# Kernel optimization log

Measured on AMD Instinct MI355X. Metric: run time of the kernel, lower is better.

Reference implementation:

```python
import jax, jax.numpy as jnp
import numpy as np

N_HEADS = 8
HEAD_DIM = 32
GROUPS = 32
EPS = 1e-5


def setup_inputs() -> dict:
    key = jax.random.key(0)
    ks = jax.random.split(key, 3)
    b, c, h, w = 8, 256, 32, 32
    x = jax.random.normal(ks[0], (b, c, h, w), dtype=jnp.float32)
    norm_w = jnp.ones((c,), dtype=jnp.float32)
    norm_b = jnp.zeros((c,), dtype=jnp.float32)
    qkv_w = jax.random.normal(ks[1], (3 * c, c), dtype=jnp.float32) * (c ** -0.5)
    qkv_b = jnp.zeros((3 * c,), dtype=jnp.float32)
    out_w = jax.random.normal(ks[2], (c, c), dtype=jnp.float32) * (c ** -0.5)
    out_b = jnp.zeros((c,), dtype=jnp.float32)
    return {"x": x, "norm_w": norm_w, "norm_b": norm_b,
            "qkv_w": qkv_w, "qkv_b": qkv_b, "out_w": out_w, "out_b": out_b}


def _group_norm(x, weight, bias):
    b, c, h, w = x.shape
    xr = x.reshape(b, GROUPS, -1)  # [b, 32, (c//32)*h*w]
    mu = xr.mean(axis=-1, keepdims=True)
    var = xr.var(axis=-1, keepdims=True)
    xn = ((xr - mu) * jax.lax.rsqrt(var + EPS)).reshape(b, c, h, w)
    return xn * weight[:, None, None] + bias[:, None, None]


def _conv1x1(x, w, b):
    # 1x1 conv == channel matmul
    return jnp.einsum('oc,bchw->bohw', w, x) + b[None, :, None, None]


def reference(x, norm_w, norm_b, qkv_w, qkv_b, out_w, out_b):
    b, c, h, w = x.shape
    hw = h * w
    scale = HEAD_DIM ** (-0.5)
    qkv = _conv1x1(_group_norm(x, norm_w, norm_b), qkv_w, qkv_b)  # [b, 3c, h, w]
    q, k, v = jnp.split(qkv, 3, axis=1)
    # torch reshape(b, n_heads, c//n_heads, h*w) is a raw row-major reshape
    q = q.reshape(b, N_HEADS, HEAD_DIM, hw) * scale
    k = k.reshape(b, N_HEADS, HEAD_DIM, hw)
    v = v.reshape(b, N_HEADS, HEAD_DIM, hw)
    sim = jnp.einsum('bhdi,bhdj->bhij', q, k)  # [b, heads, hw, hw]
    sim = sim - jax.lax.stop_gradient(sim.max(axis=-1, keepdims=True))
    attn = jax.nn.softmax(sim, axis=-1)
    out = jnp.einsum('bhij,bhdj->bhid', attn, v)  # [b, heads, hw, head_dim]
    # faithful to the original: raw reshape (b, heads, hw, head_dim) -> (b, c, h, w)
    out = out.reshape(b, c, h, w)
    return _conv1x1(out, out_w, out_b) + x
```

## Files before the change

### kernel.cpp

```cpp
#include <hip/hip_runtime.h>
#include <hip/hip_bf16.h>

#define NB 8
#define NC 256
#define NHW 1024

typedef unsigned short u16;
typedef unsigned int u32;
using f16x8  = __attribute__((ext_vector_type(8))) _Float16;
using f32x16 = __attribute__((ext_vector_type(16))) float;
using u32x4  = __attribute__((ext_vector_type(4))) unsigned int;
using u16x8  = __attribute__((ext_vector_type(8))) unsigned short;

static __device__ inline u16 f2h(float f) {
    _Float16 h = (_Float16)f;
    return __builtin_bit_cast(u16, h);
}
static __device__ inline float h2f(u16 u) {
    return (float)__builtin_bit_cast(_Float16, u);
}
static __device__ inline unsigned pk2(float a, float b) {
    auto r = __builtin_amdgcn_cvt_pkrtz(a, b);
    return __builtin_bit_cast(unsigned, r);
}
static __device__ inline float vsum16(const f32x16& v) {
    float s0 = (v[0] + v[1]) + (v[2] + v[3]);
    float s1 = (v[4] + v[5]) + (v[6] + v[7]);
    float s2 = (v[8] + v[9]) + (v[10] + v[11]);
    float s3 = (v[12] + v[13]) + (v[14] + v[15]);
    return (s0 + s1) + (s2 + s3);
}
static __device__ inline void gload16(const void* g, void* l) {
    __builtin_amdgcn_global_load_lds(
        (const __attribute__((address_space(1))) void*)g,
        (__attribute__((address_space(3))) void*)l, 16, 0, 0);
}
template<int B>
static __device__ inline f16x8 packP(const f32x16& p, const int h) {
    unsigned u0 = pk2(p[B + 0], p[B + 1]);
    unsigned u1 = pk2(p[B + 2], p[B + 3]);
    unsigned u2 = pk2(p[B + 4], p[B + 5]);
    unsigned u3 = pk2(p[B + 6], p[B + 7]);
    unsigned pu0 = __shfl_xor(u0, 32);
    unsigned pu1 = __shfl_xor(u1, 32);
    unsigned pu2 = __shfl_xor(u2, 32);
    unsigned pu3 = __shfl_xor(u3, 32);
    u32x4 w;
    w[0] = h ? pu2 : u0;
    w[1] = h ? pu3 : u1;
    w[2] = h ? u2 : pu0;
    w[3] = h ? u3 : pu1;
    return __builtin_bit_cast(f16x8, w);
}

#define QSCALE 0.25505412f

__global__ __launch_bounds__(256) void prep_kernel(
    const float* __restrict__ x, const float* __restrict__ qkv_w,
    const float* __restrict__ out_w, float2* __restrict__ stats,
    u16* __restrict__ Wq, u16* __restrict__ Wo)
{
    __shared__ float rs[4][2];
    const int bid = blockIdx.x, t = threadIdx.x;
    if (bid < 256) {
        const int g = bid & 31, b = bid >> 5;
        const size_t base = ((size_t)b * NC + g * 8) * NHW;
        const float4* xi = (const float4*)(x + base);
        float sum = 0.f, sq = 0.f;
#pragma unroll
        for (int i = 0; i < 8; ++i) {
            float4 v = xi[t + i * 256];
            sum += v.x + v.y + v.z + v.w;
            sq += v.x * v.x + v.y * v.y + v.z * v.z + v.w * v.w;
        }
        const int lane = t & 63, wv = t >> 6;
#pragma unroll
        for (int o = 32; o > 0; o >>= 1) {
            sum += __shfl_down(sum, o, 64);
            sq += __shfl_down(sq, o, 64);
        }
        if (lane == 0) { rs[wv][0] = sum; rs[wv][1] = sq; }
        __syncthreads();
        if (t == 0) {
            float S = rs[0][0] + rs[1][0] + rs[2][0] + rs[3][0];
            float Q = rs[0][1] + rs[1][1] + rs[2][1] + rs[3][1];
            float mu = S * (1.f / 8192.f);
            float var = Q * (1.f / 8192.f) - mu * mu;
            stats[b * 32 + g] = make_float2(mu, rsqrtf(var + 1e-5f));
        }
    } else {
        const int f4 = (bid - 256) * 256 + t;
        float4 v;
        u16* dhp;
        int e;
        if (f4 < 49152) {
            e = f4 * 4;
            v = *(const float4*)&qkv_w[e];
            if ((e >> 8) < 256) {
                v.x *= QSCALE; v.y *= QSCALE; v.z *= QSCALE; v.w *= QSCALE;
            }
            dhp = Wq;
        } else {
            e = (f4 - 49152) * 4;
            v = *(const float4*)&out_w[e];
            dhp = Wo;
        }
        ushort4 hh;
        hh.x = f2h(v.x); hh.y = f2h(v.y); hh.z = f2h(v.z); hh.w = f2h(v.w);
        *(ushort4*)&dhp[e] = hh;
    }
}

__global__ __launch_bounds__(256) void qkv_gemm_kernel(
    const u16* __restrict__ W, const float* __restrict__ x,
    const float2* __restrict__ stats,
    const float* __restrict__ gw, const float* __restrict__ gb,
    const float* __restrict__ bias,
    u16* __restrict__ qT, u16* __restrict__ kT, u16* __restrict__ vN)
{
    __shared__ __align__(16) u16 sB[2][2048];
    const int b = blockIdx.z;
    const int m0 = blockIdx.y * 128, n0 = blockIdx.x * 64;
    const int t = threadIdx.x, w = t >> 6, lane = t & 63;
    const int l31 = lane & 31, h = lane >> 5;
    const int msub = m0 + w * 32;

    const u16* War = W + (size_t)(msub + l31) * 256 + h * 8;

    const float bscale = (msub < 256) ? QSCALE : 1.0f;
    f32x16 acc[2];
#pragma unroll
    for (int r = 0; r < 16; ++r) {
        const int crow = (r & 3) + 8 * (r >> 2) + 4 * h;
        const float bv = bias[msub + crow] * bscale;
        acc[0][r] = bv; acc[1][r] = bv;
    }

    const int sn = t & 63;
    const int sw = w;
    const float* xs = x + (size_t)b * 256 * 1024 + (size_t)(sw * 8) * 1024 + n0 + sn;
    float vreg[8];
    const int woff = sn * 32 + ((sw ^ ((sn >> 1) & 3)) * 8);

#define LOADX(kcn) { _Pragma("unroll") for (int j = 0; j < 8; ++j) \
        vreg[j] = xs[(size_t)((kcn) * 32 + j) * 1024]; }
#define STAGE(kcn, buf) { \
        const int cb = (kcn) * 32 + sw * 8; \
        const float2 st = stats[b * 32 + (cb >> 3)]; \
        u32x4 pkv; \
        _Pragma("unroll") for (int jp = 0; jp < 4; ++jp) { \
            const float sc0 = gw[cb + jp * 2] * st.y; \
            const float of0 = gb[cb + jp * 2] - st.x * sc0; \
            const float sc1 = gw[cb + jp * 2 + 1] * st.y; \
            const float of1 = gb[cb + jp * 2 + 1] - st.x * sc1; \
            pkv[jp] = pk2(vreg[jp * 2] * sc0 + of0, vreg[jp * 2 + 1] * sc1 + of1); } \
        *(u32x4*)&sB[buf][woff] = pkv; }

    LOADX(0);
    STAGE(0, 0);
    __syncthreads();
    int cur = 0;
    for (int kc = 0; kc < 8; ++kc) {
        if (kc < 7) LOADX(kc + 1);
#pragma unroll
        for (int k16 = 0; k16 < 2; ++k16) {
            const f16x8 ah = *(const f16x8*)(War + kc * 32 + k16 * 16);
#pragma unroll
            for (int ns = 0; ns < 2; ++ns) {
                const int row = ns * 32 + l31;
                const int gi = ((k16 * 2 + h) ^ ((row >> 1) & 3)) * 8;
                const f16x8 bh = *(const f16x8*)&sB[cur][row * 32 + gi];
                acc[ns] = __builtin_amdgcn_mfma_f32_32x32x16_f16(ah, bh, acc[ns], 0, 0, 0);
            }
        }
        if (kc < 7) STAGE(kc + 1, cur ^ 1);
        __syncthreads();
        cur ^= 1;
    }
#undef LOADX
#undef STAGE

    const int type = msub >> 8;
    const int head = (msub >> 5) & 7;
    const int bh_ = b * 8 + head;
    if (type < 2) {
        u16* dst = type ? kT : qT;
#pragma unroll
        for (int ns = 0; ns < 2; ++ns) {
            const int n = n0 + ns * 32 + l31;
            u16* p = dst + ((size_t)bh_ * 1024 + n) * 32;
#pragma unroll
            for (int rp = 0; rp < 8; ++rp) {
                const int r = rp * 2;
                const int d = (r & 3) + 8 * (r >> 2) + 4 * h;
                *(unsigned*)&p[d] = (unsigned)f2h(acc[ns][r]) | ((unsigned)f2h(acc[ns][r + 1]) << 16);
            }
        }
    } else {
#pragma unroll
        for (int ns = 0; ns < 2; ++ns) {
            const int n = n0 + ns * 32 + l31;
#pragma unroll
            for (int r = 0; r < 16; ++r) {
                const int d = (r & 3) + 8 * (r >> 2) + 4 * h;
                vN[((size_t)bh_ * 32 + d) * 1024 + n] = f2h(acc[ns][r]);
            }
        }
    }
}

__global__ __launch_bounds__(256) void attn_mfma_kernel(
    const u16* __restrict__ qT, const u16* __restrict__ kT,
    const u16* __restrict__ vN, u16* __restrict__ ao)
{
    __shared__ __align__(16) u16 Ks[2][2048];
    __shared__ __align__(16) u16 Vs[2][2048];
    const int bid = blockIdx.x;
    const int itile = bid >> 6, bh = bid & 63;
    const int b = bh >> 3, head = bh & 7;
    const int t = threadIdx.x;
    const int lane = t & 63;
    const int w = t >> 6;
    const int l31 = lane & 31;
    const int h = lane >> 5;
    const int ibase = itile * 128 + w * 32;

    const u16* qrow = qT + ((size_t)bh * 1024 + ibase + l31) * 32;
    const f16x8 qf0 = *(const f16x8*)(qrow + h * 8);
    const f16x8 qf1 = *(const f16x8*)(qrow + 16 + h * 8);

    f32x16 out = {};
    float lsum = 0.f;

    const u16* ksrc = kT + ((size_t)bh * 1024 + (t >> 2)) * 32 + ((t & 3) ^ ((t >> 2) & 3)) * 8;
    const u16* vsrc = vN + ((size_t)bh * 32 + (t >> 3)) * 1024 + ((t & 7) ^ ((t >> 3) & 7)) * 8;
    const int wseg = w * 512;

    gload16(ksrc, &Ks[0][wseg]);
    gload16(vsrc, &Vs[0][wseg]);
    __syncthreads();
    int cur = 0;
    for (int T = 0; T < 16; ++T) {
        if (T < 15) {
            gload16(ksrc + (size_t)(T + 1) * 2048, &Ks[cur ^ 1][wseg]);
            gload16(vsrc + (T + 1) * 64, &Vs[cur ^ 1][wseg]);
        }
        const int gk0 = (h ^ (l31 & 3)) * 8;
        const int gk1 = ((2 + h) ^ (l31 & 3)) * 8;
        const f16x8 kf00 = *(const f16x8*)&Ks[cur][l31 * 32 + gk0];
        const f16x8 kf01 = *(const f16x8*)&Ks[cur][l31 * 32 + gk1];
        const f16x8 kf10 = *(const f16x8*)&Ks[cur][(32 + l31) * 32 + gk0];
        const f16x8 kf11 = *(const f16x8*)&Ks[cur][(32 + l31) * 32 + gk1];
        f32x16 sA = {}, sB = {};
        sA = __builtin_amdgcn_mfma_f32_32x32x16_f16(kf00, qf0, sA, 0, 0, 0);
        sA = __builtin_amdgcn_mfma_f32_32x32x16_f16(kf01, qf1, sA, 0, 0, 0);
        sB = __builtin_amdgcn_mfma_f32_32x32x16_f16(kf10, qf0, sB, 0, 0, 0);
        sB = __builtin_amdgcn_mfma_f32_32x32x16_f16(kf11, qf1, sB, 0, 0, 0);

#pragma unroll
        for (int r = 0; r < 16; ++r) {
            sA[r] = exp2f(sA[r]);
            sB[r] = exp2f(sB[r]);
        }
        float ps = vsum16(sA) + vsum16(sB);
        ps += __shfl_xor(ps, 32);
        lsum += ps;

        const f16x8 pf0 = packP<0>(sA, h);
        const f16x8 pf1 = packP<8>(sA, h);
        const f16x8 pf2 = packP<0>(sB, h);
        const f16x8 pf3 = packP<8>(sB, h);
        const int vx = l31 & 7;
        const f16x8 vf0 = *(const f16x8*)&Vs[cur][l31 * 64 + ((h    ) ^ vx) * 8];
        const f16x8 vf1 = *(const f16x8*)&Vs[cur][l31 * 64 + ((2 + h) ^ vx) * 8];
        const f16x8 vf2 = *(const f16x8*)&Vs[cur][l31 * 64 + ((4 + h) ^ vx) * 8];
        const f16x8 vf3 = *(const f16x8*)&Vs[cur][l31 * 64 + ((6 + h) ^ vx) * 8];
        out = __builtin_amdgcn_mfma_f32_32x32x16_f16(pf0, vf0, out, 0, 0, 0);
        out = __builtin_amdgcn_mfma_f32_32x32x16_f16(pf1, vf1, out, 0, 0, 0);
        out = __builtin_amdgcn_mfma_f32_32x32x16_f16(pf2, vf2, out, 0, 0, 0);
        out = __builtin_amdgcn_mfma_f32_32x32x16_f16(pf3, vf3, out, 0, 0, 0);
        __syncthreads();
        cur ^= 1;
    }

    const float linv = 1.f / lsum;
    const int cOut = b * 256 + head * 32 + itile * 4 + w;
    u16* og = ao + (size_t)cOut * 1024 + l31;
#pragma unroll
    for (int r = 0; r < 16; ++r) {
        const int crow = (r & 3) + 8 * (r >> 2) + 4 * h;
        const float sc = __shfl(linv, crow);
        og[crow * 32] = f2h(out[r] * sc);
    }
}

__global__ __launch_bounds__(256) void out_gemm_kernel(
    const u16* __restrict__ W, const u16* __restrict__ ao,
    const float* __restrict__ bias,
    const float* __restrict__ res, float* __restrict__ Y)
{
    __shared__ __align__(16) u16 sB[2][2048];
    const int b = blockIdx.z;
    const int m0 = blockIdx.y * 64, n0 = blockIdx.x * 64;
    const int t = threadIdx.x, w = t >> 6, lane = t & 63;
    const int l31 = lane & 31, h = lane >> 5;
    const int wm = w >> 1, wn = w & 1;
    const int msub = m0 + wm * 32;

    const u16* War = W + (size_t)(msub + l31) * 256 + h * 8;

    f32x16 acc;
#pragma unroll
    for (int r = 0; r < 16; ++r) {
        const int crow = (r & 3) + 8 * (r >> 2) + 4 * h;
        acc[r] = bias[msub + crow];
    }

    const int kL = t >> 3, pb = (t & 7) * 8;
    const u16* asrc = ao + ((size_t)b * 256 + kL) * 1024 + n0 + pb;
    u16x8 regs;

#define LOADC(kc) { regs = *(const u16x8*)(asrc + (size_t)(kc) * 32 * 1024); }
#define WRITEC(buf) { _Pragma("unroll") for (int e = 0; e < 8; ++e) { \
        const int n = pb + e; \
        const int idx = n * 32 + ((kL >> 3) ^ (n & 3)) * 8 + (kL & 7); \
        sB[buf][idx] = regs[e]; } }

    LOADC(0); WRITEC(0);
    __syncthreads();
    int cur = 0;
    for (int kc = 0; kc < 8; ++kc) {
        if (kc < 7) LOADC(kc + 1);
#pragma unroll
        for (int k16 = 0; k16 < 2; ++k16) {
            const f16x8 ah = *(const f16x8*)(War + kc * 32 + k16 * 16);
            const int gi = ((k16 * 2 + h) ^ (l31 & 3)) * 8;
            const int row = wn * 32 + l31;
            const f16x8 bh = *(const f16x8*)&sB[cur][row * 32 + gi];
            acc = __builtin_amdgcn_mfma_f32_32x32x16_f16(ah, bh, acc, 0, 0, 0);
        }
        if (kc < 7) WRITEC(cur ^ 1);
        __syncthreads();
        cur ^= 1;
    }
    const int n = n0 + wn * 32 + l31;
#pragma unroll
    for (int r = 0; r < 16; ++r) {
        const int mm = msub + (r & 3) + 8 * (r >> 2) + 4 * h;
        const size_t idx = ((size_t)b * 256 + mm) * 1024 + n;
        Y[idx] = acc[r] + res[idx];
    }
#undef LOADC
#undef WRITEC
}

extern "C" void kernel_launch(void* const* d_in, const int* in_sizes, int n_in,
                              void* d_out, int out_size, void* d_ws, size_t ws_size,
                              hipStream_t stream) {
    const float* x      = (const float*)d_in[0];
    const float* norm_w = (const float*)d_in[1];
    const float* norm_b = (const float*)d_in[2];
    const float* qkv_w  = (const float*)d_in[3];
    const float* qkv_b  = (const float*)d_in[4];
    const float* out_w  = (const float*)d_in[5];
    const float* out_b  = (const float*)d_in[6];
    float* out = (float*)d_out;

    char* p = (char*)d_ws;
    float2* stats = (float2*)p;  p += 4096;
    u16* Wq  = (u16*)p;  p += 393216 * 2;
    u16* Wo  = (u16*)p;  p += 131072 * 2;
    u16* qT  = (u16*)p;  p += 4u * 1024 * 1024;
    u16* kT  = (u16*)p;  p += 4u * 1024 * 1024;
    u16* vN  = (u16*)p;  p += 4u * 1024 * 1024;
    u16* ao  = (u16*)p;  p += 4u * 1024 * 1024;

    prep_kernel<<<512, 256, 0, stream>>>(x, qkv_w, out_w, stats, Wq, Wo);
    qkv_gemm_kernel<<<dim3(16, 6, NB), 256, 0, stream>>>(Wq, x, stats, norm_w, norm_b, qkv_b, qT, kT, vN);
    attn_mfma_kernel<<<512, 256, 0, stream>>>(qT, kT, vN, ao);
    out_gemm_kernel<<<dim3(16, 4, NB), 256, 0, stream>>>(Wo, ao, out_b, x, out);
}
```

Measured before the change: 62.31 us.

## Process two query tiles per wave in attention to reuse K/V fragments

Each wave in the attention kernel now handles two 32-row query tiles, 128 rows apart, instead of one. The K and V tiles loaded into shared memory, and the per-iteration K/V fragment reads, serve both. The grid is halved from 512 to 256 blocks, which cuts global and LDS traffic for K/V per query. The row-sum cross-half shuffle also moves out of the loop to the end. In exchange, register use roughly doubles for the accumulators, and there is only one block per CU, which gives less parallelism for hiding latency.

Result: slower. 73.76 us (+18.4%).

```diff
diff --git a/kernel.cpp b/kernel.cpp
--- a/kernel.cpp
+++ b/kernel.cpp
@@ -223,14 +223,17 @@
     const int w = t >> 6;
     const int l31 = lane & 31;
     const int h = lane >> 5;
-    const int ibase = itile * 128 + w * 32;
-
-    const u16* qrow = qT + ((size_t)bh * 1024 + ibase + l31) * 32;
-    const f16x8 qf0 = *(const f16x8*)(qrow + h * 8);
-    const f16x8 qf1 = *(const f16x8*)(qrow + 16 + h * 8);
-
-    f32x16 out = {};
-    float lsum = 0.f;
+    const int ibaseA = itile * 256 + w * 32;
+
+    const u16* qrowA = qT + ((size_t)bh * 1024 + ibaseA + l31) * 32;
+    const f16x8 qf0a = *(const f16x8*)(qrowA + h * 8);
+    const f16x8 qf1a = *(const f16x8*)(qrowA + 16 + h * 8);
+    const u16* qrowB = qrowA + 128 * 32;
+    const f16x8 qf0b = *(const f16x8*)(qrowB + h * 8);
+    const f16x8 qf1b = *(const f16x8*)(qrowB + 16 + h * 8);
+
+    f32x16 outA = {}, outB = {};
+    float lsumA = 0.f, lsumB = 0.f;
 
     const u16* ksrc = kT + ((size_t)bh * 1024 + (t >> 2)) * 32 + ((t & 3) ^ ((t >> 2) & 3)) * 8;
     const u16* vsrc = vN + ((size_t)bh * 32 + (t >> 3)) * 1024 + ((t & 7) ^ ((t >> 3) & 7)) * 8;
@@ -247,50 +250,76 @@
         }
         const int gk0 = (h ^ (l31 & 3)) * 8;
         const int gk1 = ((2 + h) ^ (l31 & 3)) * 8;
-        const f16x8 kf00 = *(const f16x8*)&Ks[cur][l31 * 32 + gk0];
-        const f16x8 kf01 = *(const f16x8*)&Ks[cur][l31 * 32 + gk1];
-        const f16x8 kf10 = *(const f16x8*)&Ks[cur][(32 + l31) * 32 + gk0];
-        const f16x8 kf11 = *(const f16x8*)&Ks[cur][(32 + l31) * 32 + gk1];
-        f32x16 sA = {}, sB = {};
-        sA = __builtin_amdgcn_mfma_f32_32x32x16_f16(kf00, qf0, sA, 0, 0, 0);
-        sA = __builtin_amdgcn_mfma_f32_32x32x16_f16(kf01, qf1, sA, 0, 0, 0);
-        sB = __builtin_amdgcn_mfma_f32_32x32x16_f16(kf10, qf0, sB, 0, 0, 0);
-        sB = __builtin_amdgcn_mfma_f32_32x32x16_f16(kf11, qf1, sB, 0, 0, 0);
-
-#pragma unroll
-        for (int r = 0; r < 16; ++r) {
-            sA[r] = exp2f(sA[r]);
-            sB[r] = exp2f(sB[r]);
-        }
-        float ps = vsum16(sA) + vsum16(sB);
-        ps += __shfl_xor(ps, 32);
-        lsum += ps;
-
-        const f16x8 pf0 = packP<0>(sA, h);
-        const f16x8 pf1 = packP<8>(sA, h);
-        const f16x8 pf2 = packP<0>(sB, h);
-        const f16x8 pf3 = packP<8>(sB, h);
         const int vx = l31 & 7;
         const f16x8 vf0 = *(const f16x8*)&Vs[cur][l31 * 64 + ((h    ) ^ vx) * 8];
         const f16x8 vf1 = *(const f16x8*)&Vs[cur][l31 * 64 + ((2 + h) ^ vx) * 8];
         const f16x8 vf2 = *(const f16x8*)&Vs[cur][l31 * 64 + ((4 + h) ^ vx) * 8];
         const f16x8 vf3 = *(const f16x8*)&Vs[cur][l31 * 64 + ((6 + h) ^ vx) * 8];
-        out = __builtin_amdgcn_mfma_f32_32x32x16_f16(pf0, vf0, out, 0, 0, 0);
-        out = __builtin_amdgcn_mfma_f32_32x32x16_f16(pf1, vf1, out, 0, 0, 0);
-        out = __builtin_amdgcn_mfma_f32_32x32x16_f16(pf2, vf2, out, 0, 0, 0);
-        out = __builtin_amdgcn_mfma_f32_32x32x16_f16(pf3, vf3, out, 0, 0, 0);
+
+        {
+            const f16x8 kf00 = *(const f16x8*)&Ks[cur][l31 * 32 + gk0];
+            const f16x8 kf01 = *(const f16x8*)&Ks[cur][l31 * 32 + gk1];
+            f32x16 sa = {}, sb = {};
+            sa = __builtin_amdgcn_mfma_f32_32x32x16_f16(kf00, qf0a, sa, 0, 0, 0);
+            sa = __builtin_amdgcn_mfma_f32_32x32x16_f16(kf01, qf1a, sa, 0, 0, 0);
+            sb = __builtin_amdgcn_mfma_f32_32x32x16_f16(kf00, qf0b, sb, 0, 0, 0);
+            sb = __builtin_amdgcn_mfma_f32_32x32x16_f16(kf01, qf1b, sb, 0, 0, 0);
+#pragma unroll
+            for (int r = 0; r < 16; ++r) {
+                sa[r] = exp2f(sa[r]);
+                sb[r] = exp2f(sb[r]);
+            }
+            lsumA += vsum16(sa);
+            lsumB += vsum16(sb);
+            const f16x8 pa0 = packP<0>(sa, h);
+            const f16x8 pa1 = packP<8>(sa, h);
+            const f16x8 pb0 = packP<0>(sb, h);
+            const f16x8 pb1 = packP<8>(sb, h);
+            outA = __builtin_amdgcn_mfma_f32_32x32x16_f16(pa0, vf0, outA, 0, 0, 0);
+            outA = __builtin_amdgcn_mfma_f32_32x32x16_f16(pa1, vf1, outA, 0, 0, 0);
+            outB = __builtin_amdgcn_mfma_f32_32x32x16_f16(pb0, vf0, outB, 0, 0, 0);
+            outB = __builtin_amdgcn_mfma_f32_32x32x16_f16(pb1, vf1, outB, 0, 0, 0);
+        }
+        {
+            const f16x8 kf10 = *(const f16x8*)&Ks[cur][(32 + l31) * 32 + gk0];
+            const f16x8 kf11 = *(const f16x8*)&Ks[cur][(32 + l31) * 32 + gk1];
+            f32x16 ta = {}, tb = {};
+            ta = __builtin_amdgcn_mfma_f32_32x32x16_f16(kf10, qf0a, ta, 0, 0, 0);
+            ta = __builtin_amdgcn_mfma_f32_32x32x16_f16(kf11, qf1a, ta, 0, 0, 0);
+            tb = __builtin_amdgcn_mfma_f32_32x32x16_f16(kf10, qf0b, tb, 0, 0, 0);
+            tb = __builtin_amdgcn_mfma_f32_32x32x16_f16(kf11, qf1b, tb, 0, 0, 0);
+#pragma unroll
+            for (int r = 0; r < 16; ++r) {
+                ta[r] = exp2f(ta[r]);
+                tb[r] = exp2f(tb[r]);
+            }
+            lsumA += vsum16(ta);
+            lsumB += vsum16(tb);
+            const f16x8 pa2 = packP<0>(ta, h);
+            const f16x8 pa3 = packP<8>(ta, h);
+            const f16x8 pb2 = packP<0>(tb, h);
+            const f16x8 pb3 = packP<8>(tb, h);
+            outA = __builtin_amdgcn_mfma_f32_32x32x16_f16(pa2, vf2, outA, 0, 0, 0);
+            outA = __builtin_amdgcn_mfma_f32_32x32x16_f16(pa3, vf3, outA, 0, 0, 0);
+            outB = __builtin_amdgcn_mfma_f32_32x32x16_f16(pb2, vf2, outB, 0, 0, 0);
+            outB = __builtin_amdgcn_mfma_f32_32x32x16_f16(pb3, vf3, outB, 0, 0, 0);
+        }
         __syncthreads();
         cur ^= 1;
     }
 
-    const float linv = 1.f / lsum;
-    const int cOut = b * 256 + head * 32 + itile * 4 + w;
-    u16* og = ao + (size_t)cOut * 1024 + l31;
+    lsumA += __shfl_xor(lsumA, 32);
+    lsumB += __shfl_xor(lsumB, 32);
+    const float linvA = 1.f / lsumA;
+    const float linvB = 1.f / lsumB;
+    const int cOutA = b * 256 + head * 32 + itile * 8 + w;
+    u16* ogA = ao + (size_t)cOutA * 1024 + l31;
+    u16* ogB = ogA + (size_t)4 * 1024;
 #pragma unroll
     for (int r = 0; r < 16; ++r) {
         const int crow = (r & 3) + 8 * (r >> 2) + 4 * h;
-        const float sc = __shfl(linv, crow);
-        og[crow * 32] = f2h(out[r] * sc);
+        ogA[crow * 32] = f2h(outA[r] * __shfl(linvA, crow));
+        ogB[crow * 32] = f2h(outB[r] * __shfl(linvB, crow));
     }
 }
 
@@ -377,6 +406,6 @@
 
     prep_kernel<<<512, 256, 0, stream>>>(x, qkv_w, out_w, stats, Wq, Wo);
     qkv_gemm_kernel<<<dim3(16, 6, NB), 256, 0, stream>>>(Wq, x, stats, norm_w, norm_b, qkv_b, qT, kT, vN);
-    attn_mfma_kernel<<<512, 256, 0, stream>>>(qT, kT, vN, ao);
+    attn_mfma_kernel<<<256, 256, 0, stream>>>(qT, kT, vN, ao);
     out_gemm_kernel<<<dim3(16, 4, NB), 256, 0, stream>>>(Wo, ao, out_b, x, out);
 }
```

## Split attention over key halves and merge partials in output GEMM

Applied to the files above, without the earlier changes.

Attention blocks now each process half of the key tiles, doubling the grid to 1024 blocks. Each block writes unnormalized fp32 partial outputs and row sums to workspace. The output projection kernel loads both halves, sums them, normalizes and converts to fp16 while staging into shared memory. This raises parallelism in the attention stage at the cost of much larger intermediate memory traffic and extra work in the GEMM load path.

Result: slower. 65.35 us (+4.9%).

```diff
diff --git a/kernel.cpp b/kernel.cpp
--- a/kernel.cpp
+++ b/kernel.cpp
@@ -211,13 +211,15 @@
 
 __global__ __launch_bounds__(256) void attn_mfma_kernel(
     const u16* __restrict__ qT, const u16* __restrict__ kT,
-    const u16* __restrict__ vN, u16* __restrict__ ao)
+    const u16* __restrict__ vN, float* __restrict__ pout,
+    float* __restrict__ pl)
 {
     __shared__ __align__(16) u16 Ks[2][2048];
     __shared__ __align__(16) u16 Vs[2][2048];
     const int bid = blockIdx.x;
-    const int itile = bid >> 6, bh = bid & 63;
-    const int b = bh >> 3, head = bh & 7;
+    const int jh = bid >> 9;
+    const int rem = bid & 511;
+    const int itile = rem >> 6, bh = rem & 63;
     const int t = threadIdx.x;
     const int lane = t & 63;
     const int w = t >> 6;
@@ -235,13 +237,15 @@
     const u16* ksrc = kT + ((size_t)bh * 1024 + (t >> 2)) * 32 + ((t & 3) ^ ((t >> 2) & 3)) * 8;
     const u16* vsrc = vN + ((size_t)bh * 32 + (t >> 3)) * 1024 + ((t & 7) ^ ((t >> 3) & 7)) * 8;
     const int wseg = w * 512;
-
-    gload16(ksrc, &Ks[0][wseg]);
-    gload16(vsrc, &Vs[0][wseg]);
+    const int T0 = jh * 8;
+
+    gload16(ksrc + (size_t)T0 * 2048, &Ks[0][wseg]);
+    gload16(vsrc + T0 * 64, &Vs[0][wseg]);
     __syncthreads();
     int cur = 0;
-    for (int T = 0; T < 16; ++T) {
-        if (T < 15) {
+    for (int Ti = 0; Ti < 8; ++Ti) {
+        const int T = T0 + Ti;
+        if (Ti < 7) {
             gload16(ksrc + (size_t)(T + 1) * 2048, &Ks[cur ^ 1][wseg]);
             gload16(vsrc + (T + 1) * 64, &Vs[cur ^ 1][wseg]);
         }
@@ -262,9 +266,7 @@
             sA[r] = exp2f(sA[r]);
             sB[r] = exp2f(sB[r]);
         }
-        float ps = vsum16(sA) + vsum16(sB);
-        ps += __shfl_xor(ps, 32);
-        lsum += ps;
+        lsum += vsum16(sA) + vsum16(sB);
 
         const f16x8 pf0 = packP<0>(sA, h);
         const f16x8 pf1 = packP<8>(sA, h);
@@ -283,20 +285,20 @@
         cur ^= 1;
     }
 
-    const float linv = 1.f / lsum;
-    const int cOut = b * 256 + head * 32 + itile * 4 + w;
-    u16* og = ao + (size_t)cOut * 1024 + l31;
+    lsum += __shfl_xor(lsum, 32);
+    const size_t pbase = (size_t)(jh * 64 + bh) * 1024 + ibase;
+    float* po = pout + pbase * 32 + l31;
 #pragma unroll
     for (int r = 0; r < 16; ++r) {
         const int crow = (r & 3) + 8 * (r >> 2) + 4 * h;
-        const float sc = __shfl(linv, crow);
-        og[crow * 32] = f2h(out[r] * sc);
-    }
+        po[crow * 32] = out[r];
+    }
+    if (h == 0) pl[pbase + l31] = lsum;
 }
 
 __global__ __launch_bounds__(256) void out_gemm_kernel(
-    const u16* __restrict__ W, const u16* __restrict__ ao,
-    const float* __restrict__ bias,
+    const u16* __restrict__ W, const float* __restrict__ pout,
+    const float* __restrict__ pl, const float* __restrict__ bias,
     const float* __restrict__ res, float* __restrict__ Y)
 {
     __shared__ __align__(16) u16 sB[2][2048];
@@ -317,14 +319,39 @@
     }
 
     const int kL = t >> 3, pb = (t & 7) * 8;
-    const u16* asrc = ao + ((size_t)b * 256 + kL) * 1024 + n0 + pb;
-    u16x8 regs;
-
-#define LOADC(kc) { regs = *(const u16x8*)(asrc + (size_t)(kc) * 32 * 1024); }
-#define WRITEC(buf) { _Pragma("unroll") for (int e = 0; e < 8; ++e) { \
-        const int n = pb + e; \
-        const int idx = n * 32 + ((kL >> 3) ^ (n & 3)) * 8 + (kL & 7); \
-        sB[buf][idx] = regs[e]; } }
+    const int iL = kL * 32 + ((n0 + pb) >> 5);
+    const int d0 = (n0 + pb) & 31;
+    const size_t obase0 = ((size_t)(b * 8) * 1024 + iL) * 32 + d0;
+    const size_t okc = (size_t)1024 * 32;
+    const size_t ojh = (size_t)64 * 1024 * 32;
+    const int lbase0 = (b * 8) * 1024 + iL;
+    const int lkc = 1024;
+    const int ljh = 64 * 1024;
+
+    float4 rA0, rA1, rB0, rB1;
+    float lv;
+
+#define LOADC(kc) { \
+        const float* o1 = pout + obase0 + (size_t)(kc) * okc; \
+        const float* o2 = o1 + ojh; \
+        rA0 = *(const float4*)o1; rA1 = *(const float4*)(o1 + 4); \
+        rB0 = *(const float4*)o2; rB1 = *(const float4*)(o2 + 4); \
+        lv = pl[lbase0 + (kc) * lkc] + pl[ljh + lbase0 + (kc) * lkc]; }
+#define WRITEC(buf) { \
+        const float inv = 1.f / lv; \
+        u16 mg[8]; \
+        mg[0] = f2h((rA0.x + rB0.x) * inv); \
+        mg[1] = f2h((rA0.y + rB0.y) * inv); \
+        mg[2] = f2h((rA0.z + rB0.z) * inv); \
+        mg[3] = f2h((rA0.w + rB0.w) * inv); \
+        mg[4] = f2h((rA1.x + rB1.x) * inv); \
+        mg[5] = f2h((rA1.y + rB1.y) * inv); \
+        mg[6] = f2h((rA1.z + rB1.z) * inv); \
+        mg[7] = f2h((rA1.w + rB1.w) * inv); \
+        _Pragma("unroll") for (int e = 0; e < 8; ++e) { \
+            const int n = pb + e; \
+            const int idx = n * 32 + ((kL >> 3) ^ (n & 3)) * 8 + (kL & 7); \
+            sB[buf][idx] = mg[e]; } }
 
     LOADC(0); WRITEC(0);
     __syncthreads();
@@ -373,10 +400,11 @@
     u16* qT  = (u16*)p;  p += 4u * 1024 * 1024;
     u16* kT  = (u16*)p;  p += 4u * 1024 * 1024;
     u16* vN  = (u16*)p;  p += 4u * 1024 * 1024;
-    u16* ao  = (u16*)p;  p += 4u * 1024 * 1024;
+    float* pout = (float*)p;  p += 16u * 1024 * 1024;
+    float* pl   = (float*)p;  p += 512u * 1024;
 
     prep_kernel<<<512, 256, 0, stream>>>(x, qkv_w, out_w, stats, Wq, Wo);
     qkv_gemm_kernel<<<dim3(16, 6, NB), 256, 0, stream>>>(Wq, x, stats, norm_w, norm_b, qkv_b, qT, kT, vN);
-    attn_mfma_kernel<<<512, 256, 0, stream>>>(qT, kT, vN, ao);
-    out_gemm_kernel<<<dim3(16, 4, NB), 256, 0, stream>>>(Wo, ao, out_b, x, out);
-}
+    attn_mfma_kernel<<<1024, 256, 0, stream>>>(qT, kT, vN, pout, pl);
+    out_gemm_kernel<<<dim3(16, 4, NB), 256, 0, stream>>>(Wo, pout, pl, out_b, x, out);
+}
```
